# Performance work log

Measured on AMD Instinct MI355X. Metric: run time of the kernel, lower is better.

The kernel has to match this reference:

```python
import jax, jax.numpy as jnp
import numpy as np

D = 256
H = 4
HD = D // H


def rotate_half(x):
    xp = x.reshape(x.shape[:-1] + (-1, 2))
    x1, x2 = xp[..., 0], xp[..., 1]
    return jnp.stack((-x2, x1), axis=-1).reshape(x.shape)


def apply_rope(freqs, t):
    # freqs: [2, B, 1, N, HD]; t: [B, H, N, HD]
    return t * freqs[0] + rotate_half(t) * freqs[1]


def layernorm(x, g, b, eps=1e-5):
    m = jnp.mean(x, axis=-1, keepdims=True)
    v = jnp.var(x, axis=-1, keepdims=True)
    return (x - m) * jax.lax.rsqrt(v + eps) * g + b


def ffn(z, W1, b1, g, be, W2, b2):
    h = layernorm(z @ W1 + b1, g, be)
    h = jax.nn.gelu(h, approximate=False)
    return h @ W2 + b2


def heads_split(t):
    B, N, _ = t.shape
    return t.reshape(B, N, H, HD).transpose(0, 2, 1, 3)  # [B,H,N,HD]


def heads_merge(t):
    B, h, N, hd = t.shape
    return t.transpose(0, 2, 1, 3).reshape(B, N, h * hd)


def sdpa(q, k, v):
    s = q.shape[-1] ** (-0.5)
    sim = jnp.einsum('bhid,bhjd->bhij', q, k) * s
    attn = jax.nn.softmax(sim, axis=-1)
    return jnp.einsum('bhij,bhjd->bhid', attn, v)


def self_block(x, enc, Wqkv, bqkv, Wo, bo, W1, b1, g, be, W2, b2):
    B, N, _ = x.shape
    qkv = (x @ Wqkv + bqkv).reshape(B, N, H, HD, 3).transpose(0, 2, 1, 3, 4)
    q, k, v = qkv[..., 0], qkv[..., 1], qkv[..., 2]
    q = apply_rope(enc, q)
    k = apply_rope(enc, k)
    msg = heads_merge(sdpa(q, k, v)) @ Wo + bo
    return x + ffn(jnp.concatenate([x, msg], axis=-1), W1, b1, g, be, W2, b2)


def cross_block(x0, x1, Wqk, bqk, Wv, bv, Wo, bo, W1, b1, g, be, W2, b2):
    qk0 = heads_split(x0 @ Wqk + bqk)
    qk1 = heads_split(x1 @ Wqk + bqk)
    v0 = heads_split(x0 @ Wv + bv)
    v1 = heads_split(x1 @ Wv + bv)
    s = HD ** (-0.5)
    qk0 = qk0 * (s ** 0.5)
    qk1 = qk1 * (s ** 0.5)
    sim = jnp.einsum('bhid,bhjd->bhij', qk0, qk1)
    attn01 = jax.nn.softmax(sim, axis=-1)
    attn10 = jax.nn.softmax(sim.transpose(0, 1, 3, 2), axis=-1)
    m0 = jnp.einsum('bhij,bhjd->bhid', attn01, v1)
    m1 = jnp.einsum('bhij,bhjd->bhid', attn10, v0)
    m0 = heads_merge(m0) @ Wo + bo
    m1 = heads_merge(m1) @ Wo + bo
    x0 = x0 + ffn(jnp.concatenate([x0, m0], axis=-1), W1, b1, g, be, W2, b2)
    x1 = x1 + ffn(jnp.concatenate([x1, m1], axis=-1), W1, b1, g, be, W2, b2)
    return x0, x1


def setup_inputs() -> dict:
    key = jax.random.key(0)
    ks = jax.random.split(key, 24)
    B, N = 4, 2048
    desc0 = jax.random.normal(ks[0], (B, N, D), jnp.float32)
    desc1 = jax.random.normal(ks[1], (B, N, D), jnp.float32)
    encoding0 = jax.random.uniform(ks[2], (2, B, 1, N, HD), jnp.float32)
    encoding1 = jax.random.uniform(ks[3], (2, B, 1, N, HD), jnp.float32)

    def lin(k, fin, fout):
        k1, k2 = jax.random.split(k)
        W = jax.random.normal(k1, (fin, fout), jnp.float32) * (fin ** -0.5)
        b = jax.random.normal(k2, (fout,), jnp.float32) * 0.01
        return W, b

    Wqkv, bqkv = lin(ks[4], D, 3 * D)
    Wo_s, bo_s = lin(ks[5], D, D)
    W1_s, b1_s = lin(ks[6], 2 * D, 2 * D)
    g_s = jnp.ones((2 * D,), jnp.float32)
    be_s = jnp.zeros((2 * D,), jnp.float32)
    W2_s, b2_s = lin(ks[7], 2 * D, D)
    Wqk_c, bqk_c = lin(ks[8], D, D)
    Wv_c, bv_c = lin(ks[9], D, D)
    Wo_c, bo_c = lin(ks[10], D, D)
    W1_c, b1_c = lin(ks[11], 2 * D, 2 * D)
    g_c = jnp.ones((2 * D,), jnp.float32)
    be_c = jnp.zeros((2 * D,), jnp.float32)
    W2_c, b2_c = lin(ks[12], 2 * D, D)
    return dict(desc0=desc0, desc1=desc1, encoding0=encoding0, encoding1=encoding1,
                Wqkv=Wqkv, bqkv=bqkv, Wo_s=Wo_s, bo_s=bo_s,
                W1_s=W1_s, b1_s=b1_s, g_s=g_s, be_s=be_s, W2_s=W2_s, b2_s=b2_s,
                Wqk_c=Wqk_c, bqk_c=bqk_c, Wv_c=Wv_c, bv_c=bv_c, Wo_c=Wo_c, bo_c=bo_c,
                W1_c=W1_c, b1_c=b1_c, g_c=g_c, be_c=be_c, W2_c=W2_c, b2_c=b2_c)


def reference(desc0, desc1, encoding0, encoding1,
              Wqkv, bqkv, Wo_s, bo_s, W1_s, b1_s, g_s, be_s, W2_s, b2_s,
              Wqk_c, bqk_c, Wv_c, bv_c, Wo_c, bo_c, W1_c, b1_c, g_c, be_c, W2_c, b2_c):
    d0 = self_block(desc0, encoding0, Wqkv, bqkv, Wo_s, bo_s, W1_s, b1_s, g_s, be_s, W2_s, b2_s)
    d1 = self_block(desc1, encoding1, Wqkv, bqkv, Wo_s, bo_s, W1_s, b1_s, g_s, be_s, W2_s, b2_s)
    return cross_block(d0, d1, Wqk_c, bqk_c, Wv_c, bv_c, Wo_c, bo_c, W1_c, b1_c, g_c, be_c, W2_c, b2_c)
```

## Files before the change

### kernel.cpp

```cpp
#include <hip/hip_runtime.h>
#include <math.h>

#define BB 4
#define HH 4
#define NN 2048
#define DD 256
#define HDIM 64
#define NTOK 8192
#define NTOK2 16384

typedef __attribute__((ext_vector_type(8))) __bf16 bf16x8;
typedef __attribute__((ext_vector_type(8))) unsigned short ushort8;
typedef __attribute__((ext_vector_type(4))) float floatx4;
typedef __attribute__((ext_vector_type(4))) short short4v;

union U8 { ushort8 u; bf16x8 b; };
union U4 { unsigned int u[2]; unsigned long long l; short4v s; };

#define MFMA16(a, b, c) __builtin_amdgcn_mfma_f32_16x16x16bf16_1k(a, b, c, 0, 0, 0)

__device__ __forceinline__ unsigned short f2bf(float x) {
    unsigned int u = __float_as_uint(x);
    u += 0x7FFF + ((u >> 16) & 1);
    return (unsigned short)(u >> 16);
}
__device__ __forceinline__ float bf2f(unsigned short u) {
    return __uint_as_float(((unsigned int)u) << 16);
}
__device__ __forceinline__ unsigned int pkbf(float a, float b) {
    return ((__float_as_uint(a) + 0x8000u) >> 16) |
           ((__float_as_uint(b) + 0x8000u) & 0xFFFF0000u);
}

struct WTab {
    const float* w[7];
    unsigned short* o[7];
    int K[7];
    int N[7];
    int st[7];
    int t0[8];
};

__global__ __launch_bounds__(256) void wtrans(WTab tab)
{
    __shared__ float lds[32][33];
    const int t = threadIdx.x;
    int bid = blockIdx.x;
    int s = 0;
    while (bid >= tab.t0[s + 1]) s++;
    const int ti = bid - tab.t0[s];
    const int K = tab.K[s], N = tab.N[s], st = tab.st[s];
    const int tx = ti % (N / 32), ty = ti / (N / 32);
    const int k0 = ty * 32, n0 = tx * 32;
    const float* W = tab.w[s];
    unsigned short* Wt = tab.o[s];

    {
        int r = t >> 3, c = (t & 7) * 4;
        float4 a = *(const float4*)&W[(size_t)(k0 + r) * N + n0 + c];
        lds[r][c] = a.x; lds[r][c+1] = a.y; lds[r][c+2] = a.z; lds[r][c+3] = a.w;
    }
    __syncthreads();
    {
        int n = t >> 3, kq = (t & 7) * 4;
        ushort4 p;
        p.x = f2bf(lds[kq+0][n]); p.y = f2bf(lds[kq+1][n]);
        p.z = f2bf(lds[kq+2][n]); p.w = f2bf(lds[kq+3][n]);
        *(ushort4*)&Wt[(size_t)(n0 + n) * st + k0 + kq] = p;
    }
}

__global__ __launch_bounds__(256) void wfuse(
    const float* __restrict__ Wo_s, const float* __restrict__ W1_s,
    unsigned short* __restrict__ o_s,
    const float* __restrict__ Wo_c, const float* __restrict__ W1_c,
    unsigned short* __restrict__ o_c)
{
    __shared__ float wo[32][33];
    __shared__ float w1[32][68];
    const int t = threadIdx.x;
    const int bid = blockIdx.x;
    const int seg = bid >> 6, ti_ = bid & 63;
    const int i0 = (ti_ >> 3) * 32, n0 = (ti_ & 7) * 64;
    const float* Wo  = seg ? Wo_c : Wo_s;
    const float* W1b = (seg ? W1_c : W1_s) + 256 * 512;
    unsigned short* out = seg ? o_c : o_s;
    const int ti = t >> 3, tn = t & 7;

    float acc[8] = {};
    for (int jc = 0; jc < 256; jc += 32) {
        {
            int r = t >> 3, c = (t & 7) * 4;
            *(float4*)&wo[r][c] = *(const float4*)&Wo[(size_t)(i0 + r) * 256 + jc + c];
            int c8 = (t & 7) * 8;
            *(float4*)&w1[r][c8]     = *(const float4*)&W1b[(size_t)(jc + r) * 512 + n0 + c8];
            *(float4*)&w1[r][c8 + 4] = *(const float4*)&W1b[(size_t)(jc + r) * 512 + n0 + c8 + 4];
        }
        __syncthreads();
        #pragma unroll
        for (int j = 0; j < 32; j++) {
            float a = wo[ti][j];
            #pragma unroll
            for (int e = 0; e < 8; e++) acc[e] += a * w1[j][tn * 8 + e];
        }
        __syncthreads();
    }
    #pragma unroll
    for (int e = 0; e < 8; e++)
        out[(size_t)(n0 + tn * 8 + e) * 512 + 256 + i0 + ti] = f2bf(acc[e]);
}

__global__ __launch_bounds__(256) void bfuse(
    const float* bo_s, const float* W1_s, const float* b1_s, float* bs,
    const float* bo_c, const float* W1_c, const float* b1_c, float* bc)
{
    const int seg = blockIdx.x >> 1, half = blockIdx.x & 1;
    const int n = half * 256 + threadIdx.x;
    const float* bo  = seg ? bo_c : bo_s;
    const float* W1b = (seg ? W1_c : W1_s) + 256 * 512;
    const float* b1  = seg ? b1_c : b1_s;
    float* out       = seg ? bc : bs;
    float a = b1[n];
    for (int j = 0; j < 256; j++) a += bo[j] * W1b[(size_t)j * 512 + n];
    out[n] = a;
}

__global__ __launch_bounds__(256) void gemm128(
    const unsigned short* __restrict__ A, int lda,
    const unsigned short* __restrict__ Wt, int K,
    const float* __restrict__ bias, const float* __restrict__ bias2, int mode,
    unsigned short* outH0, unsigned short* outH1, unsigned short* outH2,
    int ldc)
{
    __shared__ __align__(16) unsigned short As[128 * 40];
    __shared__ __align__(16) unsigned short Bs[128 * 40];
    const int t = threadIdx.x;
    const int w = t >> 6, lane = t & 63, quad = lane >> 4, l15 = lane & 15;
    const int m0 = blockIdx.y * 128, n0 = blockIdx.x * 128;
    const int wm = (w >> 1) * 64, wn = (w & 1) * 64;
    const int sr = t >> 1, sc = (t & 1) * 16;

    const unsigned short* Ap = A  + (size_t)(m0 + sr) * lda + sc;
    const unsigned short* Bp = Wt + (size_t)(n0 + sr) * K   + sc;

    ushort8 pa0 = *(const ushort8*)(Ap);
    ushort8 pa1 = *(const ushort8*)(Ap + 8);
    ushort8 pb0 = *(const ushort8*)(Bp);
    ushort8 pb1 = *(const ushort8*)(Bp + 8);

    floatx4 acc[4][4];
    #pragma unroll
    for (int i = 0; i < 4; i++)
        #pragma unroll
        for (int j = 0; j < 4; j++) acc[i][j] = (floatx4){0.f, 0.f, 0.f, 0.f};

    const int nk = K >> 5;
    for (int kk = 0; kk < nk; kk++) {
        *(ushort8*)&As[sr * 40 + sc]     = pa0;
        *(ushort8*)&As[sr * 40 + sc + 8] = pa1;
        *(ushort8*)&Bs[sr * 40 + sc]     = pb0;
        *(ushort8*)&Bs[sr * 40 + sc + 8] = pb1;
        __syncthreads();
        if (kk + 1 < nk) {
            int ko = (kk + 1) * 32;
            pa0 = *(const ushort8*)(Ap + ko);
            pa1 = *(const ushort8*)(Ap + ko + 8);
            pb0 = *(const ushort8*)(Bp + ko);
            pb1 = *(const ushort8*)(Bp + ko + 8);
        }
        U8 af[4], bf[4];
        #pragma unroll
        for (int i = 0; i < 4; i++)
            af[i].u = *(const ushort8*)&As[(wm + i * 16 + l15) * 40 + quad * 8];
        #pragma unroll
        for (int j = 0; j < 4; j++)
            bf[j].u = *(const ushort8*)&Bs[(wn + j * 16 + l15) * 40 + quad * 8];
        #pragma unroll
        for (int i = 0; i < 4; i++)
            #pragma unroll
            for (int j = 0; j < 4; j++)
                acc[i][j] = __builtin_amdgcn_mfma_f32_16x16x32_bf16(af[i].b, bf[j].b, acc[i][j], 0, 0, 0);
        __syncthreads();
    }

    #pragma unroll
    for (int i = 0; i < 4; i++) {
        #pragma unroll
        for (int j = 0; j < 4; j++) {
            int col = n0 + wn + j * 16 + l15;
            float bv = (mode == 2 && col >= 256) ? bias2[col & 255] : bias[col];
            #pragma unroll
            for (int r = 0; r < 4; r++) {
                int grow = m0 + wm + i * 16 + quad * 4 + r;
                float v = acc[i][j][r] + bv;
                if (mode == 1) {
                    outH0[(size_t)grow * ldc + col] = f2bf(v);
                } else if (mode == 2) {
                    int cc = col & 255;
                    int h = cc >> 6, d = cc & 63;
                    int ds = grow >> 13, b = (grow >> 11) & 3, n = grow & 2047;
                    int bh = ds * 16 + b * 4 + h;
                    if (col < 256)
                        outH0[((size_t)bh * NN + n) * HDIM + d] = f2bf(v);
                    else
                        outH1[((size_t)bh * HDIM + d) * NN + n] = f2bf(v);
                } else {
                    int sel = col % 3, cc = col / 3;
                    int h = cc >> 6, d = cc & 63;
                    int ds = grow >> 13, b = (grow >> 11) & 3, n = grow & 2047;
                    int bh = ds * 16 + b * 4 + h;
                    if (sel == 0)
                        outH0[((size_t)bh * NN + n) * HDIM + d] = f2bf(v);
                    else if (sel == 1)
                        outH1[((size_t)bh * NN + n) * HDIM + d] = f2bf(v);
                    else
                        outH2[((size_t)bh * HDIM + d) * NN + n] = f2bf(v);
                }
            }
        }
    }
}

__global__ __launch_bounds__(256) void gemm_w2(
    const unsigned short* __restrict__ A,
    const unsigned short* __restrict__ Wt,
    const float* __restrict__ bias,
    float* outF, unsigned short* outH0, unsigned short* outH1,
    const float* R0, const float* R1)
{
    __shared__ __align__(16) unsigned short As[64 * 40];
    __shared__ __align__(16) unsigned short Bs[128 * 40];
    const int t = threadIdx.x;
    const int w = t >> 6, lane = t & 63, quad = lane >> 4, l15 = lane & 15;
    const int m0 = blockIdx.y * 64, n0 = blockIdx.x * 128;
    const int wn = w * 32;
    const int sar = t >> 2, sac = (t & 3) * 8;
    const int sbr = t >> 1, sbc = (t & 1) * 16;
    const int K = 512;

    const unsigned short* Ap = A  + (size_t)(m0 + sar) * 512 + sac;
    const unsigned short* Bp = Wt + (size_t)(n0 + sbr) * K   + sbc;

    ushort8 pa  = *(const ushort8*)(Ap);
    ushort8 pb0 = *(const ushort8*)(Bp);
    ushort8 pb1 = *(const ushort8*)(Bp + 8);

    floatx4 acc[4][2];
    #pragma unroll
    for (int i = 0; i < 4; i++)
        #pragma unroll
        for (int j = 0; j < 2; j++) acc[i][j] = (floatx4){0.f, 0.f, 0.f, 0.f};

    const int nk = K >> 5;
    for (int kk = 0; kk < nk; kk++) {
        *(ushort8*)&As[sar * 40 + sac]     = pa;
        *(ushort8*)&Bs[sbr * 40 + sbc]     = pb0;
        *(ushort8*)&Bs[sbr * 40 + sbc + 8] = pb1;
        __syncthreads();
        if (kk + 1 < nk) {
            int ko = (kk + 1) * 32;
            pa  = *(const ushort8*)(Ap + ko);
            pb0 = *(const ushort8*)(Bp + ko);
            pb1 = *(const ushort8*)(Bp + ko + 8);
        }
        U8 af[4], bf[2];
        #pragma unroll
        for (int i = 0; i < 4; i++)
            af[i].u = *(const ushort8*)&As[(i * 16 + l15) * 40 + quad * 8];
        #pragma unroll
        for (int j = 0; j < 2; j++)
            bf[j].u = *(const ushort8*)&Bs[(wn + j * 16 + l15) * 40 + quad * 8];
        #pragma unroll
        for (int i = 0; i < 4; i++)
            #pragma unroll
            for (int j = 0; j < 2; j++)
                acc[i][j] = __builtin_amdgcn_mfma_f32_16x16x32_bf16(af[i].b, bf[j].b, acc[i][j], 0, 0, 0);
        __syncthreads();
    }

    #pragma unroll
    for (int i = 0; i < 4; i++) {
        #pragma unroll
        for (int j = 0; j < 2; j++) {
            int col = n0 + wn + j * 16 + l15;
            float bv = bias[col];
            #pragma unroll
            for (int r = 0; r < 4; r++) {
                int grow = m0 + i * 16 + quad * 4 + r;
                const float* R = (grow < NTOK) ? R0 : R1;
                float vv = acc[i][j][r] + bv + R[(size_t)(grow & 8191) * 256 + col];
                outF[(size_t)grow * 256 + col] = vv;
                if (outH0) outH0[(size_t)grow * 256 + col] = f2bf(vv);
                if (outH1) outH1[(size_t)grow * 512 + col] = f2bf(vv);
            }
        }
    }
}

__global__ __launch_bounds__(256) void rope_k(unsigned short* __restrict__ qb,
                                              unsigned short* __restrict__ kb,
                                              const float* __restrict__ enc0,
                                              const float* __restrict__ enc1)
{
    int i = blockIdx.x * 256 + threadIdx.x;
    int dp = (i & 31) * 2;
    int n  = (i >> 5) & (NN - 1);
    int h  = (i >> 16) & 3;
    int b  = (i >> 18) & 3;
    int ds = (i >> 20) & 1;
    int bf = (i >> 21) & 1;
    unsigned short* tq = (bf ? kb : qb) +
        (((size_t)(ds * 16 + b * 4 + h)) * NN + n) * HDIM + dp;
    const float* e0 = (ds ? enc1 : enc0) + ((size_t)b * NN + n) * HDIM + dp;
    const float* e1 = e0 + (size_t)BB * NN * HDIM;
    float x0 = bf2f(tq[0]), x1 = bf2f(tq[1]);
    float y0 = x0 * e0[0] - x1 * e1[0];
    float y1 = x1 * e0[1] + x0 * e1[1];
    tq[0] = f2bf(y0); tq[1] = f2bf(y1);
}

__global__ __launch_bounds__(256) void flash_attn(
    const unsigned short* __restrict__ Q, const unsigned short* __restrict__ K,
    const unsigned short* __restrict__ V, unsigned short* __restrict__ O,
    int ldo, int kvx, float qscale)
{
    __shared__ __align__(16) unsigned short Ks[128 * 72];
    __shared__ __align__(16) unsigned short Vt[64 * 136];

    const int t    = threadIdx.x;
    const int w    = t >> 6;
    const int lane = t & 63;
    const int quad = lane >> 4;
    const int l15  = lane & 15;
    const int bh   = blockIdx.y;
    const int kbh  = bh ^ kvx;
    const int q0   = blockIdx.x * 64;

    const unsigned short* Qb  = Q + (size_t)bh  * NN * HDIM;
    const unsigned short* Kb  = K + (size_t)kbh * NN * HDIM;
    const unsigned short* VTb = V + (size_t)kbh * NN * HDIM;

    const int krf = t >> 3, kcf = (t & 7) * 8;
    const int vrf = t >> 4, vcf = (t & 15) * 8;

    const int qrow = q0 + w * 16 + l15;
    bf16x8 qf0, qf1;
    {
        U8 r0, r1, x0, x1;
        r0.u = *(const ushort8*)&Qb[(size_t)qrow * HDIM + quad * 8];
        r1.u = *(const ushort8*)&Qb[(size_t)qrow * HDIM + 32 + quad * 8];
        #pragma unroll
        for (int j = 0; j < 8; j++) {
            x0.u[j] = f2bf(bf2f(r0.u[j]) * qscale);
            x1.u[j] = f2bf(bf2f(r1.u[j]) * qscale);
        }
        qf0 = x0.b; qf1 = x1.b;
    }

    floatx4 o[4];
    #pragma unroll
    for (int c = 0; c < 4; c++) o[c] = (floatx4){0.f, 0.f, 0.f, 0.f};
    float m = -1e30f, l = 0.f;

    ushort8 ka[4], va[4];
    #pragma unroll
    for (int i = 0; i < 4; i++) {
        ka[i] = *(const ushort8*)&Kb[(size_t)(krf + 32 * i) * HDIM + kcf];
        va[i] = *(const ushort8*)&VTb[(size_t)(vrf + 16 * i) * NN + vcf];
    }

    for (int j0 = 0; j0 < NN; j0 += 128) {
        #pragma unroll
        for (int i = 0; i < 4; i++) {
            *(ushort8*)&Ks[(krf + 32 * i) * 72 + kcf]  = ka[i];
            *(ushort8*)&Vt[(vrf + 16 * i) * 136 + vcf] = va[i];
        }
        __syncthreads();
        if (j0 + 128 < NN) {
            int jn = j0 + 128;
            #pragma unroll
            for (int i = 0; i < 4; i++) {
                ka[i] = *(const ushort8*)&Kb[(size_t)(jn + krf + 32 * i) * HDIM + kcf];
                va[i] = *(const ushort8*)&VTb[(size_t)(vrf + 16 * i) * NN + jn + vcf];
            }
        }

        floatx4 s[8];
        #pragma unroll
        for (int t8 = 0; t8 < 8; t8++) {
            U8 k0, k1;
            k0.u = *(const ushort8*)&Ks[(t8 * 16 + l15) * 72 + quad * 8];
            k1.u = *(const ushort8*)&Ks[(t8 * 16 + l15) * 72 + 32 + quad * 8];
            floatx4 z = (floatx4){0.f, 0.f, 0.f, 0.f};
            z = __builtin_amdgcn_mfma_f32_16x16x32_bf16(k0.b, qf0, z, 0, 0, 0);
            z = __builtin_amdgcn_mfma_f32_16x16x32_bf16(k1.b, qf1, z, 0, 0, 0);
            s[t8] = z;
        }

        float mx = s[0][0];
        #pragma unroll
        for (int t8 = 0; t8 < 8; t8++)
            #pragma unroll
            for (int r = 0; r < 4; r++) mx = fmaxf(mx, s[t8][r]);
        mx = fmaxf(mx, __shfl_xor(mx, 16, 64));
        mx = fmaxf(mx, __shfl_xor(mx, 32, 64));
        if (__ballot(mx > m)) {
            float mn = fmaxf(m, mx);
            float al = exp2f(m - mn);
            m = mn;
            l *= al;
            #pragma unroll
            for (int c = 0; c < 4; c++)
                #pragma unroll
                for (int r = 0; r < 4; r++) o[c][r] *= al;
        }
        float rs = 0.f;
        #pragma unroll
        for (int t8 = 0; t8 < 8; t8++)
            #pragma unroll
            for (int r = 0; r < 4; r++) {
                float p = exp2f(s[t8][r] - m);
                s[t8][r] = p;
                rs += p;
            }
        rs += __shfl_xor(rs, 16, 64);
        rs += __shfl_xor(rs, 32, 64);
        l += rs;

        short4v pf[8];
        #pragma unroll
        for (int t8 = 0; t8 < 8; t8++) {
            U4 pk;
            pk.u[0] = pkbf(s[t8][0], s[t8][1]);
            pk.u[1] = pkbf(s[t8][2], s[t8][3]);
            pf[t8] = pk.s;
        }

        #pragma unroll
        for (int c = 0; c < 4; c++) {
            #pragma unroll
            for (int t8 = 0; t8 < 8; t8++) {
                U4 vf;
                vf.l = *(const unsigned long long*)
                    &Vt[(c * 16 + l15) * 136 + t8 * 16 + quad * 4];
                o[c] = MFMA16(vf.s, pf[t8], o[c]);
            }
        }
        __syncthreads();
    }

    const int ds = bh >> 4, b = (bh >> 2) & 3, h = bh & 3;
    const int q = q0 + w * 16 + l15;
    const size_t row = (size_t)ds * NTOK + b * NN + q;
    float inv = 1.f / l;
    #pragma unroll
    for (int c = 0; c < 4; c++) {
        ushort4 pk;
        pk.x = f2bf(o[c][0] * inv);
        pk.y = f2bf(o[c][1] * inv);
        pk.z = f2bf(o[c][2] * inv);
        pk.w = f2bf(o[c][3] * inv);
        *(ushort4*)&O[row * ldo + h * HDIM + c * 16 + quad * 4] = pk;
    }
}

__global__ __launch_bounds__(256) void ln_gelu(
    unsigned short* __restrict__ hb, const float* __restrict__ g,
    const float* __restrict__ be)
{
    __shared__ float r1[4], r2[4];
    const int t = threadIdx.x;
    const size_t row = blockIdx.x;
    unsigned short* ip = hb + row * 512;
    float x0 = bf2f(ip[t]), x1 = bf2f(ip[t + 256]);
    float s = x0 + x1, ss = x0 * x0 + x1 * x1;
    #pragma unroll
    for (int o = 32; o > 0; o >>= 1) { s += __shfl_down(s, o); ss += __shfl_down(ss, o); }
    if ((t & 63) == 0) { r1[t >> 6] = s; r2[t >> 6] = ss; }
    __syncthreads();
    float S  = r1[0] + r1[1] + r1[2] + r1[3];
    float SS = r2[0] + r2[1] + r2[2] + r2[3];
    float mean = S * (1.f / 512.f);
    float var  = SS * (1.f / 512.f) - mean * mean;
    float inv  = rsqrtf(var + 1e-5f);
    float y0 = (x0 - mean) * inv * g[t]       + be[t];
    float y1 = (x1 - mean) * inv * g[t + 256] + be[t + 256];
    ip[t]       = f2bf(0.5f * y0 * (1.f + erff(y0 * 0.70710678f)));
    ip[t + 256] = f2bf(0.5f * y1 * (1.f + erff(y1 * 0.70710678f)));
}

__global__ __launch_bounds__(256) void copy_to_cat(
    const float* __restrict__ s0, const float* __restrict__ s1,
    unsigned short* __restrict__ cat)
{
    int i = blockIdx.x * 256 + threadIdx.x;
    int row = i >> 6, c4 = (i & 63) * 4;
    const float* s = (row < NTOK) ? s0 : s1;
    float4 a = *(const float4*)&s[(size_t)(row & 8191) * 256 + c4];
    ushort4 p = { f2bf(a.x), f2bf(a.y), f2bf(a.z), f2bf(a.w) };
    *(ushort4*)&cat[(size_t)row * 512 + c4] = p;
}

extern "C" void kernel_launch(void* const* d_in, const int* in_sizes, int n_in,
                              void* d_out, int out_size, void* d_ws, size_t ws_size,
                              hipStream_t stream)
{
    const float* desc0 = (const float*)d_in[0];
    const float* desc1 = (const float*)d_in[1];
    const float* enc0  = (const float*)d_in[2];
    const float* enc1  = (const float*)d_in[3];
    const float* Wqkv  = (const float*)d_in[4];  const float* bqkv  = (const float*)d_in[5];
    const float* Wo_s  = (const float*)d_in[6];  const float* bo_s  = (const float*)d_in[7];
    const float* W1_s  = (const float*)d_in[8];  const float* b1_s  = (const float*)d_in[9];
    const float* g_s   = (const float*)d_in[10]; const float* be_s  = (const float*)d_in[11];
    const float* W2_s  = (const float*)d_in[12]; const float* b2_s  = (const float*)d_in[13];
    const float* Wqk_c = (const float*)d_in[14]; const float* bqk_c = (const float*)d_in[15];
    const float* Wv_c  = (const float*)d_in[16]; const float* bv_c  = (const float*)d_in[17];
    const float* Wo_c  = (const float*)d_in[18]; const float* bo_c  = (const float*)d_in[19];
    const float* W1_c  = (const float*)d_in[20]; const float* b1_c  = (const float*)d_in[21];
    const float* g_c   = (const float*)d_in[22]; const float* be_c  = (const float*)d_in[23];
    const float* W2_c  = (const float*)d_in[24]; const float* b2_c  = (const float*)d_in[25];

    char* ws = (char*)d_ws;
    unsigned short* wt  = (unsigned short*)ws;
    unsigned short* qb  = (unsigned short*)(ws + 2490368);
    unsigned short* kb  = (unsigned short*)(ws + 10878976);
    unsigned short* vb  = (unsigned short*)(ws + 27656192);
    unsigned short* cat = (unsigned short*)(ws + 36044800);
    unsigned short* hb  = (unsigned short*)(ws + 52822016);
    unsigned short* dbf = (unsigned short*)(ws + 86376448);

    unsigned short* t_qkv  = wt;
    float*          bias_s = (float*)(wt + 196608);
    unsigned short* t_w1s  = wt + 262144;
    unsigned short* t_w2s  = wt + 524288;
    unsigned short* t_wqkc = wt + 655360;
    float*          bias_c = (float*)(wt + 786432);
    unsigned short* t_w1c  = wt + 851968;
    unsigned short* t_w2c  = wt + 1114112;

    float* outF = (float*)d_out;

    dim3 blk(256);

    WTab tab;
    tab.w[0] = Wqkv;  tab.o[0] = t_qkv;          tab.K[0] = 256; tab.N[0] = 768; tab.st[0] = 256;
    tab.w[1] = W1_s;  tab.o[1] = t_w1s;          tab.K[1] = 256; tab.N[1] = 512; tab.st[1] = 512;
    tab.w[2] = W2_s;  tab.o[2] = t_w2s;          tab.K[2] = 512; tab.N[2] = 256; tab.st[2] = 512;
    tab.w[3] = Wqk_c; tab.o[3] = t_wqkc;         tab.K[3] = 256; tab.N[3] = 256; tab.st[3] = 256;
    tab.w[4] = Wv_c;  tab.o[4] = t_wqkc + 65536; tab.K[4] = 256; tab.N[4] = 256; tab.st[4] = 256;
    tab.w[5] = W1_c;  tab.o[5] = t_w1c;          tab.K[5] = 256; tab.N[5] = 512; tab.st[5] = 512;
    tab.w[6] = W2_c;  tab.o[6] = t_w2c;          tab.K[6] = 512; tab.N[6] = 256; tab.st[6] = 512;
    int acc_t = 0;
    for (int s = 0; s < 7; s++) {
        tab.t0[s] = acc_t;
        acc_t += (tab.K[s] / 32) * (tab.N[s] / 32);
    }
    tab.t0[7] = acc_t;
    hipLaunchKernelGGL(wtrans, dim3(acc_t), blk, 0, stream, tab);
    hipLaunchKernelGGL(wfuse, dim3(128), blk, 0, stream,
                       Wo_s, W1_s, t_w1s, Wo_c, W1_c, t_w1c);
    hipLaunchKernelGGL(bfuse, dim3(4), blk, 0, stream,
                       bo_s, W1_s, b1_s, bias_s, bo_c, W1_c, b1_c, bias_c);

    auto g128 = [&](const unsigned short* A, int lda, const unsigned short* Wtp,
                    int K, const float* bias, const float* bias2, int Nc, int mode,
                    unsigned short* oh0, unsigned short* oh1, unsigned short* oh2,
                    int ldc) {
        dim3 g(Nc / 128, NTOK2 / 128);
        hipLaunchKernelGGL(gemm128, g, blk, 0, stream,
                           A, lda, Wtp, K, bias, bias2, mode, oh0, oh1, oh2, ldc);
    };

    const float QS = 0.125f * 1.44269504088896f;

    hipLaunchKernelGGL(copy_to_cat, dim3(4096), blk, 0, stream, desc0, desc1, cat);
    g128(cat, 512, t_qkv, 256, bqkv, nullptr, 768, 3, qb, kb, vb, 0);
    hipLaunchKernelGGL(rope_k, dim3(16384), blk, 0, stream, qb, kb, enc0, enc1);
    hipLaunchKernelGGL(flash_attn, dim3(NN / 64, 32), blk, 0, stream,
                       qb, kb, vb, cat + 256, 512, 0, QS);
    g128(cat, 512, t_w1s, 512, bias_s, nullptr, 512, 1, hb, nullptr, nullptr, 512);
    hipLaunchKernelGGL(ln_gelu, dim3(NTOK2), blk, 0, stream, hb, g_s, be_s);
    hipLaunchKernelGGL(gemm_w2, dim3(2, 256), blk, 0, stream,
                       hb, t_w2s, b2_s, outF, dbf, cat, desc0, desc1);

    g128(dbf, 256, t_wqkc, 256, bqk_c, bv_c, 512, 2, qb, vb, nullptr, 0);
    hipLaunchKernelGGL(flash_attn, dim3(NN / 64, 32), blk, 0, stream,
                       qb, qb, vb, cat + 256, 512, 16, QS);
    g128(cat, 512, t_w1c, 512, bias_c, nullptr, 512, 1, hb, nullptr, nullptr, 512);
    hipLaunchKernelGGL(ln_gelu, dim3(NTOK2), blk, 0, stream, hb, g_c, be_c);
    hipLaunchKernelGGL(gemm_w2, dim3(2, 256), blk, 0, stream,
                       hb, t_w2c, b2_c, outF, nullptr, nullptr,
                       outF, outF + (size_t)NTOK * 256);
}
```

Measured before the change: 497.6 us.

## Fuse RoPE into QK GEMM epilogue and compute V as transposed GEMM

The QKV weight rows are permuted so Q and K columns are contiguous. RoPE is applied in the Q/K GEMM epilogue through a lane shuffle, which removes the separate rope kernel and its read-modify-write of Q and K. V is now produced by a separate GEMM with swapped operands (W^T times X^T), so its output columns run along tokens and the transposed V layout is written contiguously instead of with strided scatter. This adds one extra GEMM launch per attention stage and extra gathers of the encoding tensor in the epilogue.

```diff
diff --git a/kernel.cpp b/kernel.cpp
--- a/kernel.cpp
+++ b/kernel.cpp
@@ -38,6 +38,7 @@
     int K[7];
     int N[7];
     int st[7];
+    int pm[7];
     int t0[8];
 };
 
@@ -49,7 +50,7 @@
     int s = 0;
     while (bid >= tab.t0[s + 1]) s++;
     const int ti = bid - tab.t0[s];
-    const int K = tab.K[s], N = tab.N[s], st = tab.st[s];
+    const int K = tab.K[s], N = tab.N[s], st = tab.st[s], pm = tab.pm[s];
     const int tx = ti % (N / 32), ty = ti / (N / 32);
     const int k0 = ty * 32, n0 = tx * 32;
     const float* W = tab.w[s];
@@ -66,7 +67,9 @@
         ushort4 p;
         p.x = f2bf(lds[kq+0][n]); p.y = f2bf(lds[kq+1][n]);
         p.z = f2bf(lds[kq+2][n]); p.w = f2bf(lds[kq+3][n]);
-        *(ushort4*)&Wt[(size_t)(n0 + n) * st + k0 + kq] = p;
+        int na = n0 + n;
+        int row = pm ? ((na % 3) * 256 + na / 3) : na;
+        *(ushort4*)&Wt[(size_t)row * st + k0 + kq] = p;
     }
 }
 
@@ -127,10 +130,10 @@
 
 __global__ __launch_bounds__(256) void gemm128(
     const unsigned short* __restrict__ A, int lda,
-    const unsigned short* __restrict__ Wt, int K,
-    const float* __restrict__ bias, const float* __restrict__ bias2, int mode,
-    unsigned short* outH0, unsigned short* outH1, unsigned short* outH2,
-    int ldc)
+    const unsigned short* __restrict__ B, int ldb, int K,
+    const float* __restrict__ bias, int mode, int bmul,
+    unsigned short* o0, unsigned short* o1, int ldc,
+    const float* __restrict__ e0g, const float* __restrict__ e1g)
 {
     __shared__ __align__(16) unsigned short As[128 * 40];
     __shared__ __align__(16) unsigned short Bs[128 * 40];
@@ -140,8 +143,8 @@
     const int wm = (w >> 1) * 64, wn = (w & 1) * 64;
     const int sr = t >> 1, sc = (t & 1) * 16;
 
-    const unsigned short* Ap = A  + (size_t)(m0 + sr) * lda + sc;
-    const unsigned short* Bp = Wt + (size_t)(n0 + sr) * K   + sc;
+    const unsigned short* Ap = A + (size_t)(m0 + sr) * lda + sc;
+    const unsigned short* Bp = B + (size_t)(n0 + sr) * ldb + sc;
 
     ushort8 pa0 = *(const ushort8*)(Ap);
     ushort8 pa1 = *(const ushort8*)(Ap + 8);
@@ -188,33 +191,36 @@
         #pragma unroll
         for (int j = 0; j < 4; j++) {
             int col = n0 + wn + j * 16 + l15;
-            float bv = (mode == 2 && col >= 256) ? bias2[col & 255] : bias[col];
+            float bv = 0.f;
+            if (mode == 5)      bv = bias[(col & 255) * 3 + (col >> 8)];
+            else if (mode == 6) bv = bias[col & 255];
+            else if (mode == 1) bv = bias[col];
             #pragma unroll
             for (int r = 0; r < 4; r++) {
                 int grow = m0 + wm + i * 16 + quad * 4 + r;
                 float v = acc[i][j][r] + bv;
                 if (mode == 1) {
-                    outH0[(size_t)grow * ldc + col] = f2bf(v);
-                } else if (mode == 2) {
+                    o0[(size_t)grow * ldc + col] = f2bf(v);
+                } else if (mode == 0) {
+                    float vv = acc[i][j][r] + bias[grow * bmul + (bmul - 1)];
+                    int h = (grow >> 6) & 3, d = grow & 63;
+                    int ds = col >> 13, b = (col >> 11) & 3, n = col & 2047;
+                    o0[((size_t)((ds * 16 + b * 4 + h) * 64 + d)) * 2048 + n] = f2bf(vv);
+                } else if (mode == 5) {
+                    int sel = col >> 8, cc = col & 255;
+                    int h = cc >> 6, d = cc & 63;
+                    int ds = grow >> 13, b = (grow >> 11) & 3, n = grow & 2047;
+                    const float* eb = (ds ? e1g : e0g) + ((size_t)(b * 2048 + n)) * 64 + d;
+                    float p = __shfl_xor(v, 1, 64);
+                    float f0 = eb[0], f1 = eb[524288];
+                    float y = v * f0 + ((d & 1) ? p : -p) * f1;
+                    unsigned short* dst = sel ? o1 : o0;
+                    dst[(((size_t)(ds * 16 + b * 4 + h)) * 2048 + n) * 64 + d] = f2bf(y);
+                } else {
                     int cc = col & 255;
                     int h = cc >> 6, d = cc & 63;
                     int ds = grow >> 13, b = (grow >> 11) & 3, n = grow & 2047;
-                    int bh = ds * 16 + b * 4 + h;
-                    if (col < 256)
-                        outH0[((size_t)bh * NN + n) * HDIM + d] = f2bf(v);
-                    else
-                        outH1[((size_t)bh * HDIM + d) * NN + n] = f2bf(v);
-                } else {
-                    int sel = col % 3, cc = col / 3;
-                    int h = cc >> 6, d = cc & 63;
-                    int ds = grow >> 13, b = (grow >> 11) & 3, n = grow & 2047;
-                    int bh = ds * 16 + b * 4 + h;
-                    if (sel == 0)
-                        outH0[((size_t)bh * NN + n) * HDIM + d] = f2bf(v);
-                    else if (sel == 1)
-                        outH1[((size_t)bh * NN + n) * HDIM + d] = f2bf(v);
-                    else
-                        outH2[((size_t)bh * HDIM + d) * NN + n] = f2bf(v);
+                    o0[(((size_t)(ds * 16 + b * 4 + h)) * 2048 + n) * 64 + d] = f2bf(v);
                 }
             }
         }
@@ -295,28 +301,6 @@
             }
         }
     }
-}
-
-__global__ __launch_bounds__(256) void rope_k(unsigned short* __restrict__ qb,
-                                              unsigned short* __restrict__ kb,
-                                              const float* __restrict__ enc0,
-                                              const float* __restrict__ enc1)
-{
-    int i = blockIdx.x * 256 + threadIdx.x;
-    int dp = (i & 31) * 2;
-    int n  = (i >> 5) & (NN - 1);
-    int h  = (i >> 16) & 3;
-    int b  = (i >> 18) & 3;
-    int ds = (i >> 20) & 1;
-    int bf = (i >> 21) & 1;
-    unsigned short* tq = (bf ? kb : qb) +
-        (((size_t)(ds * 16 + b * 4 + h)) * NN + n) * HDIM + dp;
-    const float* e0 = (ds ? enc1 : enc0) + ((size_t)b * NN + n) * HDIM + dp;
-    const float* e1 = e0 + (size_t)BB * NN * HDIM;
-    float x0 = bf2f(tq[0]), x1 = bf2f(tq[1]);
-    float y0 = x0 * e0[0] - x1 * e1[0];
-    float y1 = x1 * e0[1] + x0 * e1[1];
-    tq[0] = f2bf(y0); tq[1] = f2bf(y1);
 }
 
 __global__ __launch_bounds__(256) void flash_attn(
@@ -530,27 +514,29 @@
     unsigned short* hb  = (unsigned short*)(ws + 52822016);
     unsigned short* dbf = (unsigned short*)(ws + 86376448);
 
-    unsigned short* t_qkv  = wt;
+    unsigned short* t_qk   = wt;
+    unsigned short* t_wv   = wt + 131072;
     float*          bias_s = (float*)(wt + 196608);
-    unsigned short* t_w1s  = wt + 262144;
-    unsigned short* t_w2s  = wt + 524288;
-    unsigned short* t_wqkc = wt + 655360;
-    float*          bias_c = (float*)(wt + 786432);
-    unsigned short* t_w1c  = wt + 851968;
-    unsigned short* t_w2c  = wt + 1114112;
+    unsigned short* t_w1s  = wt + 197632;
+    unsigned short* t_w2s  = wt + 459776;
+    unsigned short* t_wqkc = wt + 590848;
+    unsigned short* t_wvc  = wt + 656384;
+    float*          bias_c = (float*)(wt + 721920);
+    unsigned short* t_w1c  = wt + 722944;
+    unsigned short* t_w2c  = wt + 985088;
 
     float* outF = (float*)d_out;
 
     dim3 blk(256);
 
     WTab tab;
-    tab.w[0] = Wqkv;  tab.o[0] = t_qkv;          tab.K[0] = 256; tab.N[0] = 768; tab.st[0] = 256;
-    tab.w[1] = W1_s;  tab.o[1] = t_w1s;          tab.K[1] = 256; tab.N[1] = 512; tab.st[1] = 512;
-    tab.w[2] = W2_s;  tab.o[2] = t_w2s;          tab.K[2] = 512; tab.N[2] = 256; tab.st[2] = 512;
-    tab.w[3] = Wqk_c; tab.o[3] = t_wqkc;         tab.K[3] = 256; tab.N[3] = 256; tab.st[3] = 256;
-    tab.w[4] = Wv_c;  tab.o[4] = t_wqkc + 65536; tab.K[4] = 256; tab.N[4] = 256; tab.st[4] = 256;
-    tab.w[5] = W1_c;  tab.o[5] = t_w1c;          tab.K[5] = 256; tab.N[5] = 512; tab.st[5] = 512;
-    tab.w[6] = W2_c;  tab.o[6] = t_w2c;          tab.K[6] = 512; tab.N[6] = 256; tab.st[6] = 512;
+    tab.w[0] = Wqkv;  tab.o[0] = wt;     tab.K[0] = 256; tab.N[0] = 768; tab.st[0] = 256; tab.pm[0] = 1;
+    tab.w[1] = W1_s;  tab.o[1] = t_w1s;  tab.K[1] = 256; tab.N[1] = 512; tab.st[1] = 512; tab.pm[1] = 0;
+    tab.w[2] = W2_s;  tab.o[2] = t_w2s;  tab.K[2] = 512; tab.N[2] = 256; tab.st[2] = 512; tab.pm[2] = 0;
+    tab.w[3] = Wqk_c; tab.o[3] = t_wqkc; tab.K[3] = 256; tab.N[3] = 256; tab.st[3] = 256; tab.pm[3] = 0;
+    tab.w[4] = Wv_c;  tab.o[4] = t_wvc;  tab.K[4] = 256; tab.N[4] = 256; tab.st[4] = 256; tab.pm[4] = 0;
+    tab.w[5] = W1_c;  tab.o[5] = t_w1c;  tab.K[5] = 256; tab.N[5] = 512; tab.st[5] = 512; tab.pm[5] = 0;
+    tab.w[6] = W2_c;  tab.o[6] = t_w2c;  tab.K[6] = 512; tab.N[6] = 256; tab.st[6] = 512; tab.pm[6] = 0;
     int acc_t = 0;
     for (int s = 0; s < 7; s++) {
         tab.t0[s] = acc_t;
@@ -563,31 +549,35 @@
     hipLaunchKernelGGL(bfuse, dim3(4), blk, 0, stream,
                        bo_s, W1_s, b1_s, bias_s, bo_c, W1_c, b1_c, bias_c);
 
-    auto g128 = [&](const unsigned short* A, int lda, const unsigned short* Wtp,
-                    int K, const float* bias, const float* bias2, int Nc, int mode,
-                    unsigned short* oh0, unsigned short* oh1, unsigned short* oh2,
-                    int ldc) {
-        dim3 g(Nc / 128, NTOK2 / 128);
-        hipLaunchKernelGGL(gemm128, g, blk, 0, stream,
-                           A, lda, Wtp, K, bias, bias2, mode, oh0, oh1, oh2, ldc);
-    };
-
     const float QS = 0.125f * 1.44269504088896f;
 
     hipLaunchKernelGGL(copy_to_cat, dim3(4096), blk, 0, stream, desc0, desc1, cat);
-    g128(cat, 512, t_qkv, 256, bqkv, nullptr, 768, 3, qb, kb, vb, 0);
-    hipLaunchKernelGGL(rope_k, dim3(16384), blk, 0, stream, qb, kb, enc0, enc1);
+    hipLaunchKernelGGL(gemm128, dim3(4, 128), blk, 0, stream,
+                       cat, 512, t_qk, 256, 256, bqkv, 5, 0,
+                       qb, kb, 0, enc0, enc1);
+    hipLaunchKernelGGL(gemm128, dim3(128, 2), blk, 0, stream,
+                       t_wv, 256, cat, 512, 256, bqkv, 0, 3,
+                       vb, nullptr, 0, nullptr, nullptr);
     hipLaunchKernelGGL(flash_attn, dim3(NN / 64, 32), blk, 0, stream,
                        qb, kb, vb, cat + 256, 512, 0, QS);
-    g128(cat, 512, t_w1s, 512, bias_s, nullptr, 512, 1, hb, nullptr, nullptr, 512);
+    hipLaunchKernelGGL(gemm128, dim3(4, 128), blk, 0, stream,
+                       cat, 512, t_w1s, 512, 512, bias_s, 1, 0,
+                       hb, nullptr, 512, nullptr, nullptr);
     hipLaunchKernelGGL(ln_gelu, dim3(NTOK2), blk, 0, stream, hb, g_s, be_s);
     hipLaunchKernelGGL(gemm_w2, dim3(2, 256), blk, 0, stream,
                        hb, t_w2s, b2_s, outF, dbf, cat, desc0, desc1);
 
-    g128(dbf, 256, t_wqkc, 256, bqk_c, bv_c, 512, 2, qb, vb, nullptr, 0);
+    hipLaunchKernelGGL(gemm128, dim3(2, 128), blk, 0, stream,
+                       dbf, 256, t_wqkc, 256, 256, bqk_c, 6, 0,
+                       qb, nullptr, 0, nullptr, nullptr);
+    hipLaunchKernelGGL(gemm128, dim3(128, 2), blk, 0, stream,
+                       t_wvc, 256, dbf, 256, 256, bv_c, 0, 1,
+                       vb, nullptr, 0, nullptr, nullptr);
     hipLaunchKernelGGL(flash_attn, dim3(NN / 64, 32), blk, 0, stream,
                        qb, qb, vb, cat + 256, 512, 16, QS);
-    g128(cat, 512, t_w1c, 512, bias_c, nullptr, 512, 1, hb, nullptr, nullptr, 512);
+    hipLaunchKernelGGL(gemm128, dim3(4, 128), blk, 0, stream,
+                       cat, 512, t_w1c, 512, 512, bias_c, 1, 0,
+                       hb, nullptr, 512, nullptr, nullptr);
     hipLaunchKernelGGL(ln_gelu, dim3(NTOK2), blk, 0, stream, hb, g_c, be_c);
     hipLaunchKernelGGL(gemm_w2, dim3(2, 256), blk, 0, stream,
                        hb, t_w2c, b2_c, outF, nullptr, nullptr,
```

New measurement: 512.5 us. +3.0%, slower.
